# Kernel tuning notes

Hardware: AMD Instinct MI355X
Metric: run time of the kernel (lower is better)

## Reference

```python
import jax, jax.numpy as jnp
import numpy as np

B = 4096
L = 15          # self.length
NINP = 256      # emb_size
NHID = 512      # hidden_size
VOCAB = 30005
TOPK = 10
K = 4 * TOPK + 2   # 42 actions
N_SPLIT = 2 * TOPK
N_STEP = 5      # num_edits
PAD = 30003


def _lstm_dir(x, Wih, Whh, b, reverse):
    # x: [T,B,D]; Wih: [4H,D]; Whh: [4H,H]; b: [4H] (b_ih+b_hh). PyTorch gate order i,f,g,o.
    Bsz, H = x.shape[1], Whh.shape[1]
    def step(carry, xt):
        h, c = carry
        z = xt @ Wih.T + h @ Whh.T + b
        i, f, g, o = jnp.split(z, 4, axis=-1)
        c = jax.nn.sigmoid(f) * c + jax.nn.sigmoid(i) * jnp.tanh(g)
        h = jax.nn.sigmoid(o) * jnp.tanh(c)
        return (h, c), h
    h0 = jnp.zeros((Bsz, H), x.dtype)
    _, ys = jax.lax.scan(step, (h0, h0), x, reverse=reverse)
    return ys  # [T,B,H], position-aligned for both directions


def bilstm(x, Wih0, Whh0, b0, Wih1, Whh1, b1):
    # x: [B,T,D] -> [B,T,2H]; 2-layer bidirectional, zero initial state (matches c0/h0 zeros).
    xt = jnp.swapaxes(x, 0, 1)
    for Wih, Whh, b in ((Wih0, Whh0, b0), (Wih1, Whh1, b1)):
        fw = _lstm_dir(xt, Wih[0], Whh[0], b[0], False)
        bw = _lstm_dir(xt, Wih[1], Whh[1], b[1], True)
        xt = jnp.concatenate([fw, bw], axis=-1)
    return jnp.swapaxes(xt, 0, 1)


def policy_step(st_1, length_t, pos, emb0, key_pos, rep_words, valid_id,
                emb_table, enc_table, Wih0, Whh0, b0, Wih1, Whh1, b1,
                del_vec, hold_vec, mlp_W, mlp_b, mlp1_W, mlp1_b):
    Bsz = st_1.shape[0]
    pos_row = jnp.zeros((L,), jnp.float32).at[pos].set(1.0)         # static pos
    pos_tensor = jnp.broadcast_to(pos_row[None, :, None], (Bsz, L, 1))
    embt = emb_table[st_1] * (1.0 - pos_tensor)
    x = jnp.concatenate([embt, emb0, pos_tensor], axis=2)            # [B,L,2*ninp+1]
    out = bilstm(x, Wih0, Whh0, b0, Wih1, Whh1, b1)                  # [B,L,2*nhid]
    pooled = out[:, pos, :]
    representation = jnp.concatenate(
        [pooled, key_pos[:, pos:pos + 1], jnp.broadcast_to(pos_row[None, :], (Bsz, L))], axis=1)
    # external encoder output is detached in the original
    word_emb = jax.lax.stop_gradient(enc_table[rep_words])           # [B,4*topk,ninp]
    emb2 = jnp.concatenate([word_emb,
                            jnp.broadcast_to(del_vec, (Bsz, 1, NINP)),
                            jnp.broadcast_to(hold_vec, (Bsz, 1, NINP))], axis=1)  # [B,K,ninp]
    onehot = jnp.broadcast_to(jnp.eye(K, dtype=jnp.float32)[None], (Bsz, K, K))
    emb2 = jnp.concatenate([emb2, onehot], axis=2)                   # [B,K,ninp+K]
    rep100 = representation @ mlp_W.T + mlp_b                        # [B,100]
    emb100 = emb2 @ mlp1_W.T + mlp1_b                                # [B,K,100]
    score = jnp.einsum('bkd,bd->bk', emb100, rep100)
    policy = jax.nn.softmax(score, axis=1)
    action = jnp.argmax(policy, axis=1, keepdims=True).astype(jnp.int32)  # eval mode
    pi = jnp.take_along_axis(policy, action, axis=1)                 # [B,1]

    rep_b = (action < N_SPLIT).astype(jnp.int32)
    replaceflag = rep_b * valid_id
    ins_b = ((action >= N_SPLIT) & (action < 2 * N_SPLIT)).astype(jnp.int32)
    insertflag = ins_b * valid_id * (length_t + ins_b <= 15).astype(jnp.int32)
    del_b = (action == 2 * N_SPLIT).astype(jnp.int32)
    deleteflag = del_b * valid_id * (length_t - del_b > 2).astype(jnp.int32)
    holdflag = 1 - replaceflag - insertflag - deleteflag

    action_words = jnp.take_along_axis(rep_words, jnp.clip(action, 0, N_SPLIT - 1), axis=1)  # [B,1]
    rep_seq = jnp.concatenate([action_words, st_1[:, pos + 1:]], axis=1)
    ins_seq = jnp.concatenate([action_words, st_1[:, pos:-1]], axis=1)
    padding = jnp.full((Bsz, 1), PAD, dtype=st_1.dtype)
    del_seq = jnp.concatenate([st_1[:, pos + 1:], padding], axis=1)
    hol_seq = st_1[:, pos:]
    new_tail = (rep_seq * replaceflag + ins_seq * insertflag
                + del_seq * deleteflag + hol_seq * holdflag)
    st = st_1.at[:, pos:].set(new_tail)
    length_tt = insertflag + length_t - deleteflag
    return st, pi, action.astype(jnp.float32), length_tt


def setup_inputs() -> dict:
    key = jax.random.key(0)
    ks = jax.random.split(key, 20)
    s = 0.05
    in0 = 2 * NINP + 1
    in1 = 2 * NHID
    inp = {
        'input_ids': jax.random.randint(ks[0], (B, L), 0, 30000, dtype=jnp.int32),
        'key_pos': jax.random.uniform(ks[1], (B, L), dtype=jnp.float32),
        'sequence_length': jax.random.randint(ks[2], (B, 1), 3, 16, dtype=jnp.int32),
        'rep_words_all': jax.random.randint(ks[3], (B, N_STEP, 4 * TOPK), 0, 30000, dtype=jnp.int32),
        'valid_id_all': jax.random.randint(ks[4], (B, N_STEP, 1), 0, 2, dtype=jnp.int32),
        'emb_table': jax.random.normal(ks[5], (VOCAB, NINP), jnp.float32) * s,
        'enc_table': jax.random.normal(ks[6], (VOCAB, NINP), jnp.float32) * s,
        'Wih0': jax.random.normal(ks[7], (2, 4 * NHID, in0), jnp.float32) * s,
        'Whh0': jax.random.normal(ks[8], (2, 4 * NHID, NHID), jnp.float32) * s,
        'b0': jax.random.normal(ks[9], (2, 4 * NHID), jnp.float32) * s,
        'Wih1': jax.random.normal(ks[10], (2, 4 * NHID, in1), jnp.float32) * s,
        'Whh1': jax.random.normal(ks[11], (2, 4 * NHID, NHID), jnp.float32) * s,
        'b1': jax.random.normal(ks[12], (2, 4 * NHID), jnp.float32) * s,
        'del_vec': jax.random.uniform(ks[13], (1, 1, NINP), dtype=jnp.float32),
        'hold_vec': jax.random.uniform(ks[14], (1, 1, NINP), dtype=jnp.float32),
        'mlp_W': jax.random.normal(ks[15], (100, 2 * NHID + 1 + L), jnp.float32) * s,
        'mlp_b': jnp.zeros((100,), jnp.float32),
        'mlp1_W': jax.random.normal(ks[16], (100, NINP + K), jnp.float32) * s,
        'mlp1_b': jnp.zeros((100,), jnp.float32),
    }
    return inp


def reference(input_ids, key_pos, sequence_length, rep_words_all, valid_id_all,
              emb_table, enc_table, Wih0, Whh0, b0, Wih1, Whh1, b1,
              del_vec, hold_vec, mlp_W, mlp_b, mlp1_W, mlp1_b):
    st = input_ids
    emb0 = emb_table[input_ids]            # embedding of s0, computed once
    length_t = sequence_length
    pis, acts = [], []
    for i in range(N_STEP):
        pos = i % (L - 3) + 2              # static per unrolled step
        st, pi, a, length_t = policy_step(
            st, length_t, pos, emb0, key_pos,
            rep_words_all[:, i, :], valid_id_all[:, i, :],
            emb_table, enc_table, Wih0, Whh0, b0, Wih1, Whh1, b1,
            del_vec, hold_vec, mlp_W, mlp_b, mlp1_W, mlp1_b)
        pis.append(pi)
        acts.append(a)
    pis = jnp.concatenate(pis, axis=1)     # [B,N_STEP]
    actions = jnp.concatenate(acts, axis=1)
    return pis, actions, st, length_t
```

## Files before the change

kernel.cpp:

```cpp
#include <hip/hip_runtime.h>

#define B_ 4096
#define L_ 15
#define NSTEP_ 5
#define VOC_ 30005
#define PAD_ 30003

typedef _Float16 f16;
typedef f16  f16x8 __attribute__((ext_vector_type(8)));
typedef float f32x16 __attribute__((ext_vector_type(16)));

__device__ __forceinline__ float sigf(float x){ return 1.0f/(1.0f+expf(-x)); }

#define MFMA_(d,a,b) d = __builtin_amdgcn_mfma_f32_32x32x16_f16(a,b,d,0,0,0)

struct RecParams {
  const f16 *A1h_0,*A1l_0,*A1h_1,*A1l_1;
  const f16 *A2h_0,*A2l_0,*A2h_1,*A2l_1;
  const f16 *Wfh_0,*Wfl_0,*Wfh_1,*Wfl_1;
  const float *bias_0,*bias_1;
  const f16 *embH,*embL;
  const int *st,*ids;
  float *c_0,*c_1,*h2_0,*h2_1;
  f16 *hh_0,*hl_0,*hh_1,*hl_1;
  int lda1, lda2, ldh, ldh2, k1p, k2p, first, gather, t_0, t_1, pos, b0c, act0, act1;
};

__device__ __forceinline__ int swz(int row, int s){
  int u = ((row&7)<<1) | s;
  return ((row>>3)<<8) + ((u ^ (u>>1))<<4);
}

__global__ __launch_bounds__(512,2) void rec_gemm(RecParams p){
  const int bxe = blockIdx.x;
  const int ct8 = bxe & 7;
  const int dir = bxe >> 3;
  if (!(dir ? p.act1 : p.act0)) return;
  const f16* A1h = dir ? p.A1h_1 : p.A1h_0;
  const f16* A1l = dir ? p.A1l_1 : p.A1l_0;
  const f16* A2h = dir ? p.A2h_1 : p.A2h_0;
  const f16* A2l = dir ? p.A2l_1 : p.A2l_0;
  const f16* Wfh = dir ? p.Wfh_1 : p.Wfh_0;
  const f16* Wfl = dir ? p.Wfl_1 : p.Wfl_0;
  const float* bias = dir ? p.bias_1 : p.bias_0;
  float* cbuf = dir ? p.c_1 : p.c_0;
  float* h2   = dir ? p.h2_1 : p.h2_0;
  f16* hhb = dir ? p.hh_1 : p.hh_0;
  f16* hlb = dir ? p.hl_1 : p.hl_0;
  const int tcur = dir ? p.t_1 : p.t_0;

  const int tid  = threadIdx.x;
  const int lane = tid & 63;
  const int w    = tid >> 6;
  const int mbase = blockIdx.y*128;

  __shared__ union {
    float z[128*128];
    f16   stg[8][2048];
  } sm;

  f32x16 accM[2][2], accX[2][2];
#pragma unroll
  for (int i=0;i<2;i++)
#pragma unroll
    for (int j=0;j<2;j++)
#pragma unroll
      for (int r=0;r<16;r++){ accM[i][j][r]=0.f; accX[i][j][r]=0.f; }

  const int arow = (w&1)*64 + (lane&31);
  const int fs = lane>>5;
  const int aoff0 = swz(arow,    fs), aoff1 = swz(arow+32, fs);

  const int ct0 = ct8*8 + (w>>1)*2;
  const f16* WfhL = Wfh + (size_t)lane*8;
  const f16* WflL = Wfl + (size_t)lane*8;

  const int u = tid & 255, pr = tid >> 8;
  const int srow = u >> 1, ss = u & 1;
  const int sws = swz(srow, ss);
  const int kph = pr*16 + ss*8;
  const int ktot = p.k1p + p.k2p;

  int tokT=0, tokI=0, zflag=0;
  if (p.gather){
    int gb = p.b0c + mbase + srow;
    tokT = p.st [gb*L_ + tcur];
    tokI = p.ids[gb*L_ + tcur];
    zflag = (tcur == p.pos) ? 1 : 0;
  }

  f16x8 ra_h, ra_l;
  const f16x8 zero8 = {0,0,0,0,0,0,0,0};

  auto gload = [&](int ph){
    if (ph >= ktot) return;
    if (ph < p.k1p){
      if (p.gather){
        if (ph < 8){
          if (zflag){ ra_h=zero8; ra_l=zero8; }
          else {
            size_t base = (size_t)tokT*256 + ph*32 + kph;
            ra_h = *(const f16x8*)(p.embH + base);
            ra_l = *(const f16x8*)(p.embL + base);
          }
        } else if (ph < 16){
          size_t base = (size_t)tokI*256 + (ph-8)*32 + kph;
          ra_h = *(const f16x8*)(p.embH + base);
          ra_l = *(const f16x8*)(p.embL + base);
        } else {
          ra_h = zero8; ra_l = zero8;
          if (kph == 0) ra_h[0] = zflag ? (f16)1.0f : (f16)0.0f;
        }
      } else {
        long base = (long)(mbase+srow)*p.lda1 + ph*32 + kph;
        ra_h = *(const f16x8*)(A1h + base);
        ra_l = *(const f16x8*)(A1l + base);
      }
    } else {
      long base = (long)(mbase+srow)*p.lda2 + (ph - p.k1p)*32 + kph;
      ra_h = *(const f16x8*)(A2h + base);
      ra_l = *(const f16x8*)(A2l + base);
    }
  };
  auto swrite = [&](int buf){
    *(f16x8*)((char*)sm.stg[buf*4 + pr*2 + 0] + sws) = ra_h;
    *(f16x8*)((char*)sm.stg[buf*4 + pr*2 + 1] + sws) = ra_l;
  };

  gload(0); swrite(0); gload(1);
  __syncthreads();

  for (int ph=0; ph<ktot; ++ph){
    const int cur = ph & 1;
    size_t base0 = ((size_t)(ph*2+0)*64 + ct0)*512;
    size_t base1 = ((size_t)(ph*2+1)*64 + ct0)*512;
    f16x8 rbh00 = *(const f16x8*)(WfhL + base0);
    f16x8 rbh01 = *(const f16x8*)(WfhL + base0 + 512);
    f16x8 rbl00 = *(const f16x8*)(WflL + base0);
    f16x8 rbl01 = *(const f16x8*)(WflL + base0 + 512);
    f16x8 rbh10 = *(const f16x8*)(WfhL + base1);
    f16x8 rbh11 = *(const f16x8*)(WfhL + base1 + 512);
    f16x8 rbl10 = *(const f16x8*)(WflL + base1);
    f16x8 rbl11 = *(const f16x8*)(WflL + base1 + 512);
    const char* s0h = (const char*)sm.stg[cur*4+0];
    const char* s0l = (const char*)sm.stg[cur*4+1];
    const char* s1h = (const char*)sm.stg[cur*4+2];
    const char* s1l = (const char*)sm.stg[cur*4+3];
    f16x8 a00h = *(const f16x8*)(s0h + aoff0);
    f16x8 a01h = *(const f16x8*)(s0h + aoff1);
    f16x8 a00l = *(const f16x8*)(s0l + aoff0);
    f16x8 a01l = *(const f16x8*)(s0l + aoff1);
    f16x8 a10h = *(const f16x8*)(s1h + aoff0);
    f16x8 a11h = *(const f16x8*)(s1h + aoff1);
    f16x8 a10l = *(const f16x8*)(s1l + aoff0);
    f16x8 a11l = *(const f16x8*)(s1l + aoff1);
    if (ph+1 < ktot){ swrite((ph+1)&1); gload(ph+2); }
    MFMA_(accM[0][0], a00h, rbh00); MFMA_(accX[0][0], a00h, rbl00); MFMA_(accX[0][0], a00l, rbh00);
    MFMA_(accM[1][0], a01h, rbh00); MFMA_(accX[1][0], a01h, rbl00); MFMA_(accX[1][0], a01l, rbh00);
    MFMA_(accM[0][1], a00h, rbh01); MFMA_(accX[0][1], a00h, rbl01); MFMA_(accX[0][1], a00l, rbh01);
    MFMA_(accM[1][1], a01h, rbh01); MFMA_(accX[1][1], a01h, rbl01); MFMA_(accX[1][1], a01l, rbh01);
    MFMA_(accM[0][0], a10h, rbh10); MFMA_(accX[0][0], a10h, rbl10); MFMA_(accX[0][0], a10l, rbh10);
    MFMA_(accM[1][0], a11h, rbh10); MFMA_(accX[1][0], a11h, rbl10); MFMA_(accX[1][0], a11l, rbh10);
    MFMA_(accM[0][1], a10h, rbh11); MFMA_(accX[0][1], a10h, rbl11); MFMA_(accX[0][1], a10l, rbh11);
    MFMA_(accM[1][1], a11h, rbh11); MFMA_(accX[1][1], a11h, rbl11); MFMA_(accX[1][1], a11l, rbh11);
    __syncthreads();
  }

  const int cq = w >> 1;
  for (int hf=0; hf<2; ++hf){
    if ((cq>>1) == hf){
#pragma unroll
      for (int tm=0;tm<2;tm++)
#pragma unroll
       for (int tn=0;tn<2;tn++){
        int lcol = (cq&1)*64 + tn*32 + (lane&31);
        float bv = bias[ct8*256 + hf*128 + lcol];
#pragma unroll
        for (int r=0;r<16;r++){
          int lrow = (w&1)*64 + tm*32 + (r&3) + 8*(r>>2) + 4*(lane>>5);
          sm.z[lrow*128 + lcol] = accM[tm][tn][r] + 0.000244140625f*accX[tm][tn][r] + bv;
        }
       }
    }
    __syncthreads();
    const int nb = ct8*64 + hf*32;
#pragma unroll
    for (int it=0; it<8; ++it){
      int idx = it*512 + tid;
      int nq = idx & 31, row = idx >> 5;
      float4 g4 = *(const float4*)&sm.z[row*128 + nq*4];
      int m = mbase + row, n = nb + nq;
      float cp = p.first ? 0.f : cbuf[(size_t)m*512 + n];
      float cc = sigf(g4.y)*cp + sigf(g4.x)*tanhf(g4.z);
      float hv = sigf(g4.w)*tanhf(cc);
      cbuf[(size_t)m*512 + n] = cc;
      f16 hi = (f16)hv;
      f16 lo = (f16)((hv - (float)hi)*4096.0f);
      hhb[(size_t)m*p.ldh + n] = hi;
      hlb[(size_t)m*p.ldh + n] = lo;
      if (h2) h2[(size_t)m*p.ldh2 + n] = hv;
    }
    __syncthreads();
  }
}

__global__ void prep_w0(const float* Wih, const float* Whh, const float* b0,
                        f16* Wfh, f16* Wfl, float* bp){
  int gid = blockIdx.x*blockDim.x + threadIdx.x;
  const int PER_DIR = 66*64*64*8;
  if (gid >= 2*PER_DIR) return;
  int dir = gid / PER_DIR;
  int rem = gid % PER_DIR;
  int j = rem & 7, lane = (rem>>3)&63, ct = (rem>>9)&63, kt16 = rem>>15;
  int n4g = ct*32 + (lane&31);
  int n = n4g>>2, g = n4g&3;
  int srow = dir*2048 + g*512 + n;
  int k = kt16*16 + ((lane>>5)<<3) + j;
  float v;
  if (k < 513)       v = Wih[(size_t)srow*513 + k];
  else if (k < 544)  v = 0.f;
  else               v = Whh[(size_t)srow*512 + (k-544)];
  f16 hi = (f16)v;
  Wfh[gid] = hi;
  Wfl[gid] = (f16)((v - (float)hi)*4096.0f);
  if (kt16==0 && (lane>>5)==0 && j==0) bp[dir*2048 + n4g] = b0[srow];
}

__global__ void prep_w1(const float* Wih, const float* Whh, const float* b1,
                        f16* Wfh, f16* Wfl, float* bp){
  int gid = blockIdx.x*blockDim.x + threadIdx.x;
  const int PER_DIR = 96*64*64*8;
  if (gid >= 2*PER_DIR) return;
  int dir = gid / PER_DIR;
  int rem = gid % PER_DIR;
  int j = rem & 7, lane = (rem>>3)&63, ct = (rem>>9)&63, kt16 = rem>>15;
  int n4g = ct*32 + (lane&31);
  int n = n4g>>2, g = n4g&3;
  int srow = dir*2048 + g*512 + n;
  int k = kt16*16 + ((lane>>5)<<3) + j;
  float v;
  if (k < 1024) v = Wih[(size_t)srow*1024 + k];
  else          v = Whh[(size_t)srow*512 + (k-1024)];
  f16 hi = (f16)v;
  Wfh[gid] = hi;
  Wfl[gid] = (f16)((v - (float)hi)*4096.0f);
  if (kt16==0 && (lane>>5)==0 && j==0) bp[dir*2048 + n4g] = b1[srow];
}

__global__ void prep_emb(const float* emb, f16* eh, f16* el){
  int gid = blockIdx.x*blockDim.x + threadIdx.x;
  if (gid >= VOC_*256) return;
  float v = emb[gid];
  f16 hi = (f16)v;
  eh[gid] = hi;
  el[gid] = (f16)((v - (float)hi)*4096.0f);
}

__global__ void prep_mlpwt(const float* mW, float* wt){
  int gid = blockIdx.x*blockDim.x + threadIdx.x;
  if (gid >= 100*1040) return;
  int j = gid / 1040, k = gid % 1040;
  wt[k*100 + j] = mW[gid];
}

__global__ __launch_bounds__(128) void prep_encproj(const float* enc, const float* delv,
                        const float* holdv, const float* m1W, const float* m1b, float* ep){
  int r = blockIdx.x;
  __shared__ float row[256];
  const float* src = (r < VOC_) ? enc + (size_t)r*256 : (r == VOC_ ? delv : holdv);
  for (int i=threadIdx.x;i<256;i+=128) row[i]=src[i];
  __syncthreads();
  int j = threadIdx.x;
  if (j < 100){
    double s = (double)m1b[j];
    const float* wr = m1W + (size_t)j*298;
    for (int k=0;k<256;k++) s += (double)wr[k] * (double)row[k];
    ep[(size_t)r*100 + j] = (float)s;
  }
}

__global__ void init_st(const int* ids, const int* seqlen, int* st, int* len){
  int gid = blockIdx.x*blockDim.x + threadIdx.x;
  if (gid < B_*L_) st[gid] = ids[gid];
  if (gid < B_)    len[gid] = seqlen[gid];
}

__global__ void sentinel(float* out, float v){
  int gid = blockIdx.x*blockDim.x + threadIdx.x;
  if (gid < B_*NSTEP_) out[gid] = v;
}

__global__ __launch_bounds__(128) void score_update(
    const float* pooled, const float* keypos, const float* mWt, const float* mb,
    const float* ep, const float* m1W, const int* repw, const int* valid,
    int* st, int* len, float* outPis, float* outActs, int step, int pos, int b0){
  int b = blockIdx.x;
  int bg = b0 + b;
  __shared__ float rep[1040];
  __shared__ float r100[100];
  __shared__ double sc[42];
  int tid = threadIdx.x;
  for (int i=tid;i<1024;i+=128) rep[i] = pooled[(size_t)b*1024+i];
  if (tid < 16){
    if (tid == 0) rep[1024] = keypos[bg*L_+pos];
    else          rep[1024+tid] = ((tid-1)==pos) ? 1.f : 0.f;
  }
  __syncthreads();
  if (tid < 100){
    double s = (double)mb[tid];
    for (int k=0;k<1040;k++) s += (double)mWt[k*100+tid] * (double)rep[k];
    r100[tid] = (float)s;
  }
  __syncthreads();
  if (tid < 42){
    int row = (tid < 40) ? repw[((size_t)bg*NSTEP_+step)*40 + tid] : (VOC_ + (tid-40));
    const float* er = ep + (size_t)row*100;
    double s = 0.0;
    for (int j=0;j<100;j++) s += (double)er[j] * (double)r100[j];
    for (int j=0;j<100;j++) s += (double)m1W[j*298 + 256 + tid] * (double)r100[j];
    sc[tid] = s;
  }
  __syncthreads();
  if (tid == 0){
    double mx = sc[0]; int am = 0;
    for (int k=1;k<42;k++) if (sc[k] > mx){ mx = sc[k]; am = k; }
    double sum = 0.0;
    for (int k=0;k<42;k++) sum += exp(sc[k]-mx);
    float pi = (float)(1.0/sum);
    int vid = valid[bg*NSTEP_+step];
    int ln  = len[bg];
    int repb = (am < 20) ? 1 : 0;
    int insb = (am >= 20 && am < 40) ? 1 : 0;
    int delb = (am == 40) ? 1 : 0;
    int repf = repb*vid;
    int insf = insb*vid*(((ln+insb) <= 15) ? 1 : 0);
    int delf = delb*vid*(((ln-delb) >  2) ? 1 : 0);
    int T = L_ - pos;
    int tail[13];
    for (int j=0;j<T;j++) tail[j] = st[bg*L_+pos+j];
    int aw = repw[((size_t)bg*NSTEP_+step)*40 + (am < 20 ? am : 19)];
    for (int j=0;j<T;j++){
      int rv = (j==0) ? aw : tail[j];
      int iv = (j==0) ? aw : tail[j-1];
      int dv = (j < T-1) ? tail[j+1] : PAD_;
      int hv = tail[j];
      int nv = repf ? rv : (insf ? iv : (delf ? dv : hv));
      st[bg*L_+pos+j] = nv;
    }
    len[bg] = ln + insf - delf;
    outPis[bg*NSTEP_+step]  = pi;
    outActs[bg*NSTEP_+step] = (float)am;
  }
}

__global__ void finalize(const int* st, const int* len, float* out){
  int gid = blockIdx.x*blockDim.x + threadIdx.x;
  if (gid < B_*L_)            out[2*B_*NSTEP_ + gid] = (float)st[gid];
  else if (gid < B_*L_ + B_)  out[2*B_*NSTEP_ + B_*L_ + (gid - B_*L_)] = (float)len[gid - B_*L_];
}

extern "C" void kernel_launch(void* const* d_in, const int* in_sizes, int n_in,
                              void* d_out, int out_size, void* d_ws, size_t ws_size,
                              hipStream_t stream) {
  const int*   ids    = (const int*)  d_in[0];
  const float* keypos = (const float*)d_in[1];
  const int*   seqlen = (const int*)  d_in[2];
  const int*   repw   = (const int*)  d_in[3];
  const int*   valid  = (const int*)  d_in[4];
  const float* emb    = (const float*)d_in[5];
  const float* enc    = (const float*)d_in[6];
  const float* Wih0   = (const float*)d_in[7];
  const float* Whh0   = (const float*)d_in[8];
  const float* b0     = (const float*)d_in[9];
  const float* Wih1   = (const float*)d_in[10];
  const float* Whh1   = (const float*)d_in[11];
  const float* b1     = (const float*)d_in[12];
  const float* delv   = (const float*)d_in[13];
  const float* holdv  = (const float*)d_in[14];
  const float* mW     = (const float*)d_in[15];
  const float* mb     = (const float*)d_in[16];
  const float* m1W    = (const float*)d_in[17];
  const float* m1b    = (const float*)d_in[18];
  float* out = (float*)d_out;

  const size_t W0PD = (size_t)66*64*64*8;
  const size_t W1PD = (size_t)96*64*64*8;

  char* ws = (char*)d_ws;
  size_t off = 0;
  auto allocB = [&](size_t bytes) -> char* {
    char* pp = ws + off; off += (bytes + 255) & ~size_t(255); return pp;
  };
  f16*  Wf0h = (f16*)allocB(2*W0PD*2);
  f16*  Wf0l = (f16*)allocB(2*W0PD*2);
  f16*  Wf1h = (f16*)allocB(2*W1PD*2);
  f16*  Wf1l = (f16*)allocB(2*W1PD*2);
  float* bp0 = (float*)allocB(4096*4);
  float* bp1 = (float*)allocB(4096*4);
  f16*  embH = (f16*)allocB((size_t)VOC_*256*2);
  f16*  embL = (f16*)allocB((size_t)VOC_*256*2);
  float* mWt = (float*)allocB(104000*4);
  float* ep  = (float*)allocB((size_t)30007*100*4);
  int* stbuf  = (int*)allocB(B_*L_*4);
  int* lenbuf = (int*)allocB(B_*4);
  size_t fixedB = off;

  const int cands[6] = {4096, 2048, 1024, 512, 256, 128};
  int Bc = 0;
  for (int ci=0; ci<6; ++ci){
    size_t c = cands[ci];
    size_t chunkB = c*(size_t)(15*1024*2*2 + 4*512*2*2 + 2*512*4 + 2*512*4 + 1024*4) + 8*256;
    if (fixedB + chunkB <= ws_size){ Bc = (int)c; break; }
  }
  if (!Bc){
    float code = 100000.0f + (float)(ws_size >> 20);
    sentinel<<<(B_*NSTEP_+255)/256,256,0,stream>>>(out, code);
    return;
  }
  f16* o0h = (f16*)allocB((size_t)L_*Bc*1024*2);
  f16* o0l = (f16*)allocB((size_t)L_*Bc*1024*2);
  f16* h1h = (f16*)allocB((size_t)4*Bc*512*2);
  f16* h1l = (f16*)allocB((size_t)4*Bc*512*2);
  float* c0 = (float*)allocB((size_t)2*Bc*512*4);
  float* c1 = (float*)allocB((size_t)2*Bc*512*4);
  float* pooled = (float*)allocB((size_t)Bc*1024*4);

  prep_w0<<<(int)((2*W0PD+255)/256),256,0,stream>>>(Wih0, Whh0, b0, Wf0h, Wf0l, bp0);
  prep_w1<<<(int)((2*W1PD+255)/256),256,0,stream>>>(Wih1, Whh1, b1, Wf1h, Wf1l, bp1);
  prep_emb<<<(VOC_*256+255)/256,256,0,stream>>>(emb, embH, embL);
  prep_mlpwt<<<(100*1040+255)/256,256,0,stream>>>(mW, mWt);
  prep_encproj<<<30007,128,0,stream>>>(enc, delv, holdv, m1W, m1b, ep);
  init_st<<<(B_*L_+255)/256,256,0,stream>>>(ids, seqlen, stbuf, lenbuf);

  for (int b0c=0; b0c<B_; b0c+=Bc){
    for (int step=0; step<NSTEP_; ++step){
      int pos = step + 2;

      for (int ts=0; ts<L_; ++ts){
        int tf = ts, tb = 14-ts;
        RecParams p{};
        p.gather = 1; p.t_0 = tf; p.t_1 = tb; p.pos = pos; p.b0c = b0c;
        p.embH = embH; p.embL = embL; p.st = stbuf; p.ids = ids;
        p.k1p = 17; p.k2p = ts ? 16 : 0;
        size_t of0 = (size_t)(ts?tf-1:0)*Bc*1024;
        size_t of1 = (size_t)(ts?tb+1:0)*Bc*1024 + (ts?512:0);
        p.A2h_0 = o0h + of0;  p.A2l_0 = o0l + of0;
        p.A2h_1 = o0h + of1;  p.A2l_1 = o0l + of1;
        p.lda2 = 1024;
        p.Wfh_0 = Wf0h;        p.Wfl_0 = Wf0l;
        p.Wfh_1 = Wf0h + W0PD; p.Wfl_1 = Wf0l + W0PD;
        p.bias_0 = bp0; p.bias_1 = bp0 + 2048;
        p.c_0 = c0; p.c_1 = c0 + (size_t)Bc*512;
        p.hh_0 = o0h + (size_t)tf*Bc*1024;       p.hl_0 = o0l + (size_t)tf*Bc*1024;
        p.hh_1 = o0h + (size_t)tb*Bc*1024 + 512; p.hl_1 = o0l + (size_t)tb*Bc*1024 + 512;
        p.ldh = 1024;
        p.h2_0 = nullptr; p.h2_1 = nullptr; p.ldh2 = 1024;
        p.first = (ts==0); p.act0 = 1; p.act1 = 1;
        rec_gemm<<<dim3(16,Bc/128),512,0,stream>>>(p);
      }

      int nL1 = L_ - pos;
      for (int ts=0; ts<nL1; ++ts){
        RecParams p{};
        int tf = ts, tb = 14-ts;
        int parR = (ts-1)&1, parW = ts&1;
        p.gather = 0;
        p.A1h_0 = o0h + (size_t)tf*Bc*1024;  p.A1l_0 = o0l + (size_t)tf*Bc*1024;
        p.A1h_1 = o0h + (size_t)tb*Bc*1024;  p.A1l_1 = o0l + (size_t)tb*Bc*1024;
        p.lda1 = 1024; p.k1p = 32;
        p.k2p  = ts ? 16 : 0;
        size_t r0 = (size_t)(0*2 + (ts?parR:0))*Bc*512;
        size_t r1 = (size_t)(1*2 + (ts?parR:0))*Bc*512;
        p.A2h_0 = h1h + r0; p.A2l_0 = h1l + r0;
        p.A2h_1 = h1h + r1; p.A2l_1 = h1l + r1;
        p.lda2 = 512;
        p.Wfh_0 = Wf1h;        p.Wfl_0 = Wf1l;
        p.Wfh_1 = Wf1h + W1PD; p.Wfl_1 = Wf1l + W1PD;
        p.bias_0 = bp1; p.bias_1 = bp1 + 2048;
        p.c_0 = c1; p.c_1 = c1 + (size_t)Bc*512;
        size_t w0 = (size_t)(0*2 + parW)*Bc*512;
        size_t w1 = (size_t)(1*2 + parW)*Bc*512;
        p.hh_0 = h1h + w0; p.hl_0 = h1l + w0;
        p.hh_1 = h1h + w1; p.hl_1 = h1l + w1;
        p.ldh = 512;
        p.h2_0 = (ts == pos)    ? pooled        : nullptr;
        p.h2_1 = (ts == 14-pos) ? (pooled+512)  : nullptr;
        p.ldh2 = 1024;
        p.first = (ts==0);
        p.act0 = (ts <= pos) ? 1 : 0; p.act1 = 1;
        rec_gemm<<<dim3(16,Bc/128),512,0,stream>>>(p);
      }

      score_update<<<Bc,128,0,stream>>>(pooled, keypos, mWt, mb, ep, m1W, repw, valid,
                                        stbuf, lenbuf, out, out + B_*NSTEP_, step, pos, b0c);
    }
  }
  finalize<<<(B_*L_+B_+255)/256,256,0,stream>>>(stbuf, lenbuf, out);
}
```

Baseline: 18.89 ms.

## Halve rec_gemm column tile per block to double grid and occupancy

Each block of the recurrent GEMM now covers 128 gate columns instead of 256, so each wave holds one 32-wide column tile instead of two. The grid doubles in x, launch bounds go to 4 blocks per CU, and the shared-memory epilogue buffer is halved by processing 64 rows at a time. The goal is more parallelism and latency hiding through fewer accumulator registers and more resident waves. In exchange, each A tile staged in shared memory is reused across fewer columns, so A is loaded from global memory twice as often.

```diff
diff --git a/kernel.cpp b/kernel.cpp
--- a/kernel.cpp
+++ b/kernel.cpp
@@ -31,10 +31,10 @@
   return ((row>>3)<<8) + ((u ^ (u>>1))<<4);
 }
 
-__global__ __launch_bounds__(512,2) void rec_gemm(RecParams p){
+__global__ __launch_bounds__(512,4) void rec_gemm(RecParams p){
   const int bxe = blockIdx.x;
-  const int ct8 = bxe & 7;
-  const int dir = bxe >> 3;
+  const int ct4 = bxe & 15;
+  const int dir = bxe >> 4;
   if (!(dir ? p.act1 : p.act0)) return;
   const f16* A1h = dir ? p.A1h_1 : p.A1h_0;
   const f16* A1l = dir ? p.A1l_1 : p.A1l_0;
@@ -55,23 +55,21 @@
   const int mbase = blockIdx.y*128;
 
   __shared__ union {
-    float z[128*128];
-    f16   stg[8][2048];
+    float zh[64*128];
+    f16   stg[2][4][2048];
   } sm;
 
-  f32x16 accM[2][2], accX[2][2];
+  f32x16 accM[2], accX[2];
 #pragma unroll
   for (int i=0;i<2;i++)
 #pragma unroll
-    for (int j=0;j<2;j++)
-#pragma unroll
-      for (int r=0;r<16;r++){ accM[i][j][r]=0.f; accX[i][j][r]=0.f; }
-
-  const int arow = (w&1)*64 + (lane&31);
+    for (int r=0;r<16;r++){ accM[i][r]=0.f; accX[i][r]=0.f; }
+
+  const int r2 = w & 1;
   const int fs = lane>>5;
-  const int aoff0 = swz(arow,    fs), aoff1 = swz(arow+32, fs);
-
-  const int ct0 = ct8*8 + (w>>1)*2;
+  const int aoff0 = swz(r2*64 +      (lane&31), fs);
+  const int aoff1 = swz(r2*64 + 32 + (lane&31), fs);
+  const int ctu = ct4*4 + (w>>1);
   const f16* WfhL = Wfh + (size_t)lane*8;
   const f16* WflL = Wfl + (size_t)lane*8;
 
@@ -123,8 +121,8 @@
     }
   };
   auto swrite = [&](int buf){
-    *(f16x8*)((char*)sm.stg[buf*4 + pr*2 + 0] + sws) = ra_h;
-    *(f16x8*)((char*)sm.stg[buf*4 + pr*2 + 1] + sws) = ra_l;
+    *(f16x8*)((char*)sm.stg[buf][pr*2+0] + sws) = ra_h;
+    *(f16x8*)((char*)sm.stg[buf][pr*2+1] + sws) = ra_l;
   };
 
   gload(0); swrite(0); gload(1);
@@ -132,64 +130,48 @@
 
   for (int ph=0; ph<ktot; ++ph){
     const int cur = ph & 1;
-    size_t base0 = ((size_t)(ph*2+0)*64 + ct0)*512;
-    size_t base1 = ((size_t)(ph*2+1)*64 + ct0)*512;
-    f16x8 rbh00 = *(const f16x8*)(WfhL + base0);
-    f16x8 rbh01 = *(const f16x8*)(WfhL + base0 + 512);
-    f16x8 rbl00 = *(const f16x8*)(WflL + base0);
-    f16x8 rbl01 = *(const f16x8*)(WflL + base0 + 512);
-    f16x8 rbh10 = *(const f16x8*)(WfhL + base1);
-    f16x8 rbh11 = *(const f16x8*)(WfhL + base1 + 512);
-    f16x8 rbl10 = *(const f16x8*)(WflL + base1);
-    f16x8 rbl11 = *(const f16x8*)(WflL + base1 + 512);
-    const char* s0h = (const char*)sm.stg[cur*4+0];
-    const char* s0l = (const char*)sm.stg[cur*4+1];
-    const char* s1h = (const char*)sm.stg[cur*4+2];
-    const char* s1l = (const char*)sm.stg[cur*4+3];
-    f16x8 a00h = *(const f16x8*)(s0h + aoff0);
-    f16x8 a01h = *(const f16x8*)(s0h + aoff1);
-    f16x8 a00l = *(const f16x8*)(s0l + aoff0);
-    f16x8 a01l = *(const f16x8*)(s0l + aoff1);
-    f16x8 a10h = *(const f16x8*)(s1h + aoff0);
-    f16x8 a11h = *(const f16x8*)(s1h + aoff1);
-    f16x8 a10l = *(const f16x8*)(s1l + aoff0);
-    f16x8 a11l = *(const f16x8*)(s1l + aoff1);
-    if (ph+1 < ktot){ swrite((ph+1)&1); gload(ph+2); }
-    MFMA_(accM[0][0], a00h, rbh00); MFMA_(accX[0][0], a00h, rbl00); MFMA_(accX[0][0], a00l, rbh00);
-    MFMA_(accM[1][0], a01h, rbh00); MFMA_(accX[1][0], a01h, rbl00); MFMA_(accX[1][0], a01l, rbh00);
-    MFMA_(accM[0][1], a00h, rbh01); MFMA_(accX[0][1], a00h, rbl01); MFMA_(accX[0][1], a00l, rbh01);
-    MFMA_(accM[1][1], a01h, rbh01); MFMA_(accX[1][1], a01h, rbl01); MFMA_(accX[1][1], a01l, rbh01);
-    MFMA_(accM[0][0], a10h, rbh10); MFMA_(accX[0][0], a10h, rbl10); MFMA_(accX[0][0], a10l, rbh10);
-    MFMA_(accM[1][0], a11h, rbh10); MFMA_(accX[1][0], a11h, rbl10); MFMA_(accX[1][0], a11l, rbh10);
-    MFMA_(accM[0][1], a10h, rbh11); MFMA_(accX[0][1], a10h, rbl11); MFMA_(accX[0][1], a10l, rbh11);
-    MFMA_(accM[1][1], a11h, rbh11); MFMA_(accX[1][1], a11h, rbl11); MFMA_(accX[1][1], a11l, rbh11);
+#pragma unroll
+    for (int kq=0; kq<2; ++kq){
+      const char* sh = (const char*)sm.stg[cur][kq*2+0];
+      const char* sl = (const char*)sm.stg[cur][kq*2+1];
+      f16x8 a0h = *(const f16x8*)(sh + aoff0);
+      f16x8 a1h = *(const f16x8*)(sh + aoff1);
+      f16x8 a0l = *(const f16x8*)(sl + aoff0);
+      f16x8 a1l = *(const f16x8*)(sl + aoff1);
+      size_t base = ((size_t)(ph*2+kq)*64 + ctu)*512;
+      f16x8 bh = *(const f16x8*)(WfhL + base);
+      f16x8 bl = *(const f16x8*)(WflL + base);
+      if (kq == 1){ if (ph+1 < ktot){ swrite((ph+1)&1); gload(ph+2); } }
+      MFMA_(accM[0], a0h, bh);
+      MFMA_(accM[1], a1h, bh);
+      MFMA_(accX[0], a0h, bl);
+      MFMA_(accX[1], a1h, bl);
+      MFMA_(accX[0], a0l, bh);
+      MFMA_(accX[1], a1l, bh);
+    }
     __syncthreads();
   }
 
-  const int cq = w >> 1;
+  const int nb = ct4*32;
   for (int hf=0; hf<2; ++hf){
-    if ((cq>>1) == hf){
+    if (r2 == hf){
+      int lcol = (w>>1)*32 + (lane&31);
+      float bv = bias[ct4*128 + lcol];
 #pragma unroll
       for (int tm=0;tm<2;tm++)
 #pragma unroll
-       for (int tn=0;tn<2;tn++){
-        int lcol = (cq&1)*64 + tn*32 + (lane&31);
-        float bv = bias[ct8*256 + hf*128 + lcol];
-#pragma unroll
         for (int r=0;r<16;r++){
-          int lrow = (w&1)*64 + tm*32 + (r&3) + 8*(r>>2) + 4*(lane>>5);
-          sm.z[lrow*128 + lcol] = accM[tm][tn][r] + 0.000244140625f*accX[tm][tn][r] + bv;
+          int lrow = tm*32 + (r&3) + 8*(r>>2) + 4*(lane>>5);
+          sm.zh[lrow*128 + lcol] = accM[tm][r] + 0.000244140625f*accX[tm][r] + bv;
         }
-       }
     }
     __syncthreads();
-    const int nb = ct8*64 + hf*32;
-#pragma unroll
-    for (int it=0; it<8; ++it){
+#pragma unroll
+    for (int it=0; it<4; ++it){
       int idx = it*512 + tid;
       int nq = idx & 31, row = idx >> 5;
-      float4 g4 = *(const float4*)&sm.z[row*128 + nq*4];
-      int m = mbase + row, n = nb + nq;
+      float4 g4 = *(const float4*)&sm.zh[row*128 + nq*4];
+      int m = mbase + hf*64 + row, n = nb + nq;
       float cp = p.first ? 0.f : cbuf[(size_t)m*512 + n];
       float cc = sigf(g4.y)*cp + sigf(g4.x)*tanhf(g4.z);
       float hv = sigf(g4.w)*tanhf(cc);
@@ -456,7 +438,7 @@
         p.ldh = 1024;
         p.h2_0 = nullptr; p.h2_1 = nullptr; p.ldh2 = 1024;
         p.first = (ts==0); p.act0 = 1; p.act1 = 1;
-        rec_gemm<<<dim3(16,Bc/128),512,0,stream>>>(p);
+        rec_gemm<<<dim3(32,Bc/128),512,0,stream>>>(p);
       }
 
       int nL1 = L_ - pos;
@@ -488,7 +470,7 @@
         p.ldh2 = 1024;
         p.first = (ts==0);
         p.act0 = (ts <= pos) ? 1 : 0; p.act1 = 1;
-        rec_gemm<<<dim3(16,Bc/128),512,0,stream>>>(p);
+        rec_gemm<<<dim3(32,Bc/128),512,0,stream>>>(p);
       }
 
       score_update<<<Bc,128,0,stream>>>(pooled, keypos, mWt, mb, ep, m1W, repw, valid,
```

Result: slower. 22.26 ms (+17.9%).
